# Kernel optimization log

Measured on AMD Instinct MI355X. Metric: run time of the kernel, lower is better.

## Reference

```python
import jax, jax.numpy as jnp
import numpy as np

NUM_LAYERS = 6
DIM = 512
VOCAB = 50257
HEADS = 8
EXPERTS = 8
TOPK = 2
LN_EPS = 1e-5


def setup_inputs() -> dict:
    key = jax.random.key(0)
    ks = jax.random.split(key, 9)
    d, L, E = DIM, NUM_LAYERS, EXPERTS
    return {
        'input_ids': jax.random.randint(ks[0], (2, 1024), 0, VOCAB),
        'embed': jax.random.normal(ks[1], (VOCAB, d), dtype=jnp.float32) * 0.02,
        'qkv_w': jax.random.normal(ks[2], (L, 3 * d, d), dtype=jnp.float32) * 0.02,
        'out_w': jax.random.normal(ks[3], (L, d, d), dtype=jnp.float32) * 0.02,
        'router_w': jax.random.normal(ks[4], (L, E, d), dtype=jnp.float32) * 0.02,
        'router_b': jnp.zeros((L, E), dtype=jnp.float32),
        'w1': jax.random.normal(ks[5], (L, E, 2 * d, d), dtype=jnp.float32) * 0.02,
        'b1': jnp.zeros((L, E, 2 * d), dtype=jnp.float32),
        'w2': jax.random.normal(ks[6], (L, E, d, 2 * d), dtype=jnp.float32) * 0.02,
        'b2': jnp.zeros((L, E, d), dtype=jnp.float32),
        'ln_g': jnp.ones((L, d), dtype=jnp.float32),
        'ln_b': jnp.zeros((L, d), dtype=jnp.float32),
        'head_w': jax.random.normal(ks[7], (VOCAB, d), dtype=jnp.float32) * 0.02,
    }


def _bit_weight(w):
    # BitNet 1.58b training-mode effective weight (STE forward value):
    # scale = mean|w| per output row; w_eff = round(w/scale).clip(-1,1) * scale
    scale = jnp.clip(jnp.mean(jnp.abs(w), axis=-1, keepdims=True), 1e-5, None)
    wq = jnp.clip(jnp.round(w / scale), -1.0, 1.0)
    w_ste = jax.lax.stop_gradient(wq - w) + w
    return w_ste * scale


def _layer_norm(x, g, b):
    mu = jnp.mean(x, axis=-1, keepdims=True)
    var = jnp.mean(jnp.square(x - mu), axis=-1, keepdims=True)
    return (x - mu) * jax.lax.rsqrt(var + LN_EPS) * g + b


def _attention(x, qkv_w, out_w):
    B, Lq, D = x.shape
    hd = D // HEADS
    qkv = (x @ qkv_w.T).reshape(B, Lq, 3, HEADS, hd).transpose(2, 0, 3, 1, 4)
    q, k, v = qkv[0], qkv[1], qkv[2]  # [B,H,L,hd]
    attn = jax.nn.softmax(jnp.einsum('bhqd,bhkd->bhqk', q, k) * hd ** -0.5, axis=-1)
    o = jnp.einsum('bhqk,bhkd->bhqd', attn, v).transpose(0, 2, 1, 3).reshape(B, Lq, D)
    return o @ out_w.T


def _moe(x, rw, rb, w1, b1, w2, b2, g, beta):
    B, Lq, D = x.shape
    N = B * Lq
    xf = x.reshape(N, D)
    probs = jax.nn.softmax(xf @ rw.T + rb, axis=-1)  # [N,E]
    vals, idx = jax.lax.top_k(probs, TOPK)
    vals = vals / (jnp.sum(vals, axis=-1, keepdims=True) + 1e-8)
    # combine weights: [N,E] (top-k indices are distinct, so sum == scatter)
    cw = jnp.sum(jax.nn.one_hot(idx, EXPERTS, dtype=xf.dtype) * vals[..., None], axis=1)
    we1 = _bit_weight(w1)  # [E,2D,D]
    we2 = _bit_weight(w2)  # [E,D,2D]
    h = jax.nn.gelu(jnp.einsum('nd,efd->enf', xf, we1) + b1[:, None, :], approximate=False)
    y = jnp.einsum('enf,edf->end', h, we2) + b2[:, None, :]  # [E,N,D]
    out = jnp.einsum('ne,end->nd', cw, y)
    return _layer_norm(out + xf, g, beta).reshape(B, Lq, D)


def reference(input_ids, embed, qkv_w, out_w, router_w, router_b, w1, b1, w2, b2, ln_g, ln_b, head_w):
    x = embed[input_ids]  # [B,L,D]
    for l in range(NUM_LAYERS):
        x = x + _attention(x, qkv_w[l], out_w[l])
        x = _moe(x, router_w[l], router_b[l], w1[l], b1[l], w2[l], b2[l], ln_g[l], ln_b[l])
    return x @ head_w.T  # logits [B,L,V]
```

## Files before the change

kernel.cpp:

```cpp
#include <hip/hip_runtime.h>
#include <math.h>
#include <stdint.h>

#define NLAYER 6
#define DIMD 512
#define HEADS 8
#define HD 64
#define EXPERTS 8
#define SEQ 1024
#define NTOK 2048
#define FF 1024
#define VOCABN 50257
#define HROWS 50304

typedef __bf16 bf16;
typedef __bf16 bf16x8 __attribute__((ext_vector_type(8)));
typedef __bf16 bf16x4 __attribute__((ext_vector_type(4)));
typedef float f32x4 __attribute__((ext_vector_type(4)));

__device__ __forceinline__ void gl_lds16(const void* g, void* l) {
  __builtin_amdgcn_global_load_lds(
      (const __attribute__((address_space(1))) void*)(uintptr_t)g,
      (__attribute__((address_space(3))) void*)(uintptr_t)l, 16, 0, 0);
}

#define LDSW(row, kg) (((row) * 32) + ((((kg) ^ (((row) >> 1) & 3))) << 3))

template <int BNT>
__global__ __launch_bounds__(256) void k_mfma_gemm(
    const bf16* __restrict__ A0, const bf16* __restrict__ A1,
    const bf16* __restrict__ B0, const bf16* __restrict__ B1,
    float* __restrict__ Cf, bf16* __restrict__ Cb0, bf16* __restrict__ Cb1,
    bf16* __restrict__ Cb2, bf16* __restrict__ E0, bf16* __restrict__ E1,
    bf16* __restrict__ E2, int M, int N, int K,
    long sA, long sB, long sCf, long sCb,
    const float* __restrict__ colScale, int csStride,
    const float* __restrict__ bias, int biasStride,
    const float* __restrict__ residual, int act, int mode,
    const int* __restrict__ mLimit, const int* __restrict__ aperm,
    int outmode) {
  constexpr int NI = BNT / 32;
  __shared__ __align__(16) bf16 As[128 * 32];
  __shared__ __align__(16) bf16 Bs[BNT * 32];
  int tid = threadIdx.x;
  int z = blockIdx.z;
  int nwg = gridDim.x * gridDim.y;
  int flat = blockIdx.y * gridDim.x + blockIdx.x;
  int qq = nwg >> 3, rr = nwg & 7;
  int xcd = flat & 7, ii = flat >> 3;
  int swz = (xcd < rr ? xcd * (qq + 1) : rr * (qq + 1) + (xcd - rr) * qq) + ii;
  int m0 = (swz % gridDim.x) * 128, n0 = (swz / gridDim.x) * BNT;
  if (mLimit && m0 >= mLimit[z]) return;
  int w = tid >> 6, lane = tid & 63;
  int wm = (w >> 1) * 64, wn = (w & 1) * (16 * NI);
  int r15 = lane & 15, kg = lane >> 4;

  int pa[3] = {0, 0, 0}, pb[3] = {0, 0, 0};
  int np = 1;
  if (mode == 3) {
    np = 2; pa[1] = 1;
  } else if (mode == 5) {
    np = 3;
    pa[1] = 0; pb[1] = 1; pa[2] = 1; pb[2] = 0;
  }

  f32x4 acc[4][NI] = {};
  int srow = tid >> 2;
  int scol = (((tid & 3) ^ ((tid >> 3) & 3))) << 3;
  long arow0, arow1;
  if (aperm) {
    arow0 = aperm[z * 2048 + m0 + srow];
    arow1 = aperm[z * 2048 + m0 + 64 + srow];
  } else {
    arow0 = m0 + srow;
    arow1 = m0 + 64 + srow;
  }
  const bf16* PA[2] = {A0, A1};
  const bf16* PB[2] = {B0, B1};
  bf16* la0 = &As[tid * 8];
  bf16* la1 = &As[64 * 32 + tid * 8];
  bf16* lb0 = &Bs[tid * 8];

  for (int p = 0; p < np; ++p) {
    const bf16* Az = PA[pa[p]] + (long)z * sA;
    const bf16* Bz = PB[pb[p]] + (long)z * sB;
    const bf16* ga0 = Az + arow0 * K + scol;
    const bf16* ga1 = Az + arow1 * K + scol;
    const bf16* gb0 = Bz + (long)(n0 + srow) * K + scol;
    const bf16* gb1 = (BNT == 128) ? Bz + (long)(n0 + 64 + srow) * K + scol
                                   : nullptr;
    for (int k0 = 0; k0 < K; k0 += 32) {
      gl_lds16(ga0, la0);
      gl_lds16(ga1, la1);
      gl_lds16(gb0, lb0);
      if constexpr (BNT == 128) gl_lds16(gb1, &Bs[64 * 32 + tid * 8]);
      ga0 += 32; ga1 += 32; gb0 += 32;
      if constexpr (BNT == 128) gb1 += 32;
      __syncthreads();
      bf16x8 af[4], bfr[NI];
#pragma unroll
      for (int mi = 0; mi < 4; ++mi) {
        int rowA = wm + mi * 16 + r15;
        af[mi] = *(const bf16x8*)&As[LDSW(rowA, kg)];
      }
#pragma unroll
      for (int ni = 0; ni < NI; ++ni) {
        int rowB = wn + ni * 16 + r15;
        bfr[ni] = *(const bf16x8*)&Bs[LDSW(rowB, kg)];
      }
#pragma unroll
      for (int mi = 0; mi < 4; ++mi)
#pragma unroll
        for (int ni = 0; ni < NI; ++ni)
          acc[mi][ni] = __builtin_amdgcn_mfma_f32_16x16x32_bf16(
              af[mi], bfr[ni], acc[mi][ni], 0, 0, 0);
      __syncthreads();
    }
  }

#pragma unroll
  for (int mi = 0; mi < 4; ++mi) {
    int rbase = m0 + wm + mi * 16 + kg * 4;
#pragma unroll
    for (int ni = 0; ni < NI; ++ni) {
      int col = n0 + wn + ni * 16 + r15;
      if (col >= N) continue;
      float scl = colScale ? colScale[z * csStride + col] : 1.f;
      float bv = bias ? bias[z * biasStride + col] : 0.f;
#pragma unroll
      for (int reg = 0; reg < 4; ++reg) {
        int row = rbase + reg;
        float v = acc[mi][ni][reg] * scl + bv;
        if (act) v = 0.5f * v * (1.f + erff(v * 0.70710678118654752f));
        if (residual) v += residual[(long)row * N + col];
        if (outmode == 2) {
          int b = row >> 10, qt = row & 1023;
          if (n0 < 512) {
            float qv = v * 0.125f;
            int h = col >> 6, d = col & 63;
            long dst = ((long)(b * 8 + h)) * ((long)SEQ * HD) +
                       (long)qt * HD + d;
            bf16 h0 = (bf16)qv;
            Cb0[dst] = h0;
            Cb1[dst] = (bf16)(qv - (float)h0);
          } else if (n0 < 1024) {
            int c2 = col - 512;
            int h = c2 >> 6, d = c2 & 63;
            long dst = ((long)(b * 8 + h)) * ((long)SEQ * HD) +
                       (long)qt * HD + d;
            bf16 h0 = (bf16)v;
            Cb2[dst] = h0;
            E0[dst] = (bf16)(v - (float)h0);
          } else {
            int c2 = col - 1024;
            int h = c2 >> 6, d = c2 & 63;
            long dst = ((long)(b * 8 + h)) * ((long)HD * SEQ) +
                       (long)d * SEQ + qt;
            bf16 h0 = (bf16)v;
            E1[dst] = h0;
            E2[dst] = (bf16)(v - (float)h0);
          }
          continue;
        }
        if (Cf) Cf[z * sCf + (long)row * N + col] = v;
        if (Cb0) {
          long cib = z * sCb + (long)row * N + col;
          bf16 h0 = (bf16)v;
          Cb0[cib] = h0;
          if (Cb1) {
            float r = v - (float)h0;
            Cb1[cib] = (bf16)r;
          }
        }
      }
    }
  }
}

__global__ __launch_bounds__(256) void k_fattn(
    const bf16* __restrict__ q0b, const bf16* __restrict__ q1b,
    const bf16* __restrict__ k0b, const bf16* __restrict__ k1b,
    const bf16* __restrict__ vt0, const bf16* __restrict__ vt1,
    bf16* __restrict__ at0, bf16* __restrict__ at1) {
  __shared__ __align__(16) bf16 Ks[2][128 * 64];
  __shared__ __align__(16) bf16 Vs[2][64 * 128];
  __shared__ __align__(16) bf16 Ps[2][64 * 128];
  int tid = threadIdx.x;
  int bh = blockIdx.y;
  int q0 = blockIdx.x * 64;
  int w = tid >> 6, lane = tid & 63;
  int r15 = lane & 15, kg = lane >> 4;
  const long bhQK = (long)bh * SEQ * HD;
  const long bhV = (long)bh * HD * SEQ;

  bf16x8 qa0[2], qa1[2];
  {
    long qoff = bhQK + (long)(q0 + w * 16 + r15) * HD;
#pragma unroll
    for (int ks = 0; ks < 2; ++ks) {
      qa0[ks] = *(const bf16x8*)&q0b[qoff + ks * 32 + kg * 8];
      qa1[ks] = *(const bf16x8*)&q1b[qoff + ks * 32 + kg * 8];
    }
  }

  auto stageK = [&](int kt) {
#pragma unroll
    for (int i = 0; i < 4; ++i) {
      int L = tid + i * 256;
      int row = L >> 3, pc = L & 7;
      int gc = pc ^ (row & 7);
      long gsrc = bhQK + (long)(kt * 128 + row) * HD + gc * 8;
      gl_lds16(k0b + gsrc, &Ks[0][L * 8]);
      gl_lds16(k1b + gsrc, &Ks[1][L * 8]);
    }
  };
  auto stageV = [&](int kt) {
#pragma unroll
    for (int i = 0; i < 4; ++i) {
      int L = tid + i * 256;
      int row = L >> 4, pc = L & 15;
      int gc = pc ^ (row & 15);
      long gsrc = bhV + (long)row * SEQ + kt * 128 + gc * 8;
      gl_lds16(vt0 + gsrc, &Vs[0][L * 8]);
      gl_lds16(vt1 + gsrc, &Vs[1][L * 8]);
    }
  };
  auto computeS = [&](f32x4* sf) {
#pragma unroll
    for (int kc = 0; kc < 8; ++kc) {
      f32x4 a = {};
      int rowB = kc * 16 + r15;
#pragma unroll
      for (int ks = 0; ks < 2; ++ks) {
        int pc = (ks * 4 + kg) ^ (rowB & 7);
        bf16x8 b0 = *(const bf16x8*)&Ks[0][rowB * 64 + pc * 8];
        bf16x8 b1 = *(const bf16x8*)&Ks[1][rowB * 64 + pc * 8];
        a = __builtin_amdgcn_mfma_f32_16x16x32_bf16(qa0[ks], b0, a, 0, 0, 0);
        a = __builtin_amdgcn_mfma_f32_16x16x32_bf16(qa0[ks], b1, a, 0, 0, 0);
        a = __builtin_amdgcn_mfma_f32_16x16x32_bf16(qa1[ks], b0, a, 0, 0, 0);
      }
      sf[kc] = a;
    }
  };

  float m[4], l[4];
#pragma unroll
  for (int r = 0; r < 4; ++r) { m[r] = -1e30f; l[r] = 0.f; }
  f32x4 oacc[4] = {};

  for (int kt = 0; kt < SEQ / 128; ++kt) {
    stageK(kt);
    stageV(kt);
    __syncthreads();
    f32x4 sf[8];
    computeS(sf);
#pragma unroll
    for (int r = 0; r < 4; ++r) {
      float tm = sf[0][r];
#pragma unroll
      for (int kc = 1; kc < 8; ++kc) tm = fmaxf(tm, sf[kc][r]);
      tm = fmaxf(tm, __shfl_xor(tm, 1));
      tm = fmaxf(tm, __shfl_xor(tm, 2));
      tm = fmaxf(tm, __shfl_xor(tm, 4));
      tm = fmaxf(tm, __shfl_xor(tm, 8));
      float mn = fmaxf(m[r], tm);
      float corr = __expf(m[r] - mn);
      float s = 0.f;
#pragma unroll
      for (int kc = 0; kc < 8; ++kc) {
        float p = __expf(sf[kc][r] - mn);
        sf[kc][r] = p;
        s += p;
      }
      s += __shfl_xor(s, 1);
      s += __shfl_xor(s, 2);
      s += __shfl_xor(s, 4);
      s += __shfl_xor(s, 8);
      l[r] = l[r] * corr + s;
      m[r] = mn;
#pragma unroll
      for (int dg = 0; dg < 4; ++dg) oacc[dg][r] *= corr;
    }
#pragma unroll
    for (int kc = 0; kc < 8; ++kc) {
#pragma unroll
      for (int r = 0; r < 4; ++r) {
        float p = sf[kc][r];
        bf16 h0 = (bf16)p;
        bf16 h1 = (bf16)(p - (float)h0);
        int qrow = w * 16 + kg * 4 + r;
        int kcol = kc * 16 + r15;
        int pc = (kcol >> 3) ^ (qrow & 15);
        int addr = qrow * 128 + pc * 8 + (kcol & 7);
        Ps[0][addr] = h0;
        Ps[1][addr] = h1;
      }
    }
    bf16x8 pa0[4], pa1[4];
    int rowP = w * 16 + r15;
#pragma unroll
    for (int ks = 0; ks < 4; ++ks) {
      int pc = (ks * 4 + kg) ^ (rowP & 15);
      pa0[ks] = *(const bf16x8*)&Ps[0][rowP * 128 + pc * 8];
      pa1[ks] = *(const bf16x8*)&Ps[1][rowP * 128 + pc * 8];
    }
#pragma unroll
    for (int dg = 0; dg < 4; ++dg) {
      int rowV = dg * 16 + r15;
#pragma unroll
      for (int ks = 0; ks < 4; ++ks) {
        int pc = (ks * 4 + kg) ^ (rowV & 15);
        bf16x8 v0 = *(const bf16x8*)&Vs[0][rowV * 128 + pc * 8];
        bf16x8 v1 = *(const bf16x8*)&Vs[1][rowV * 128 + pc * 8];
        oacc[dg] = __builtin_amdgcn_mfma_f32_16x16x32_bf16(pa0[ks], v0,
                                                           oacc[dg], 0, 0, 0);
        oacc[dg] = __builtin_amdgcn_mfma_f32_16x16x32_bf16(pa0[ks], v1,
                                                           oacc[dg], 0, 0, 0);
        oacc[dg] = __builtin_amdgcn_mfma_f32_16x16x32_bf16(pa1[ks], v0,
                                                           oacc[dg], 0, 0, 0);
      }
    }
    __syncthreads();
  }

  float invl[4];
#pragma unroll
  for (int r = 0; r < 4; ++r) invl[r] = 1.f / l[r];

  int b = bh >> 3, h = bh & 7;
#pragma unroll
  for (int dg = 0; dg < 4; ++dg) {
#pragma unroll
    for (int r = 0; r < 4; ++r) {
      int qrow = q0 + w * 16 + kg * 4 + r;
      int d = dg * 16 + r15;
      long dst = ((long)(b * SEQ + qrow)) * DIMD + h * HD + d;
      float v = oacc[dg][r] * invl[r];
      bf16 h0 = (bf16)v;
      at0[dst] = h0;
      at1[dst] = (bf16)(v - (float)h0);
    }
  }
}

__global__ __launch_bounds__(256) void k_hgemm(const bf16* __restrict__ A,
                                               const bf16* __restrict__ Bt,
                                               float* __restrict__ C,
                                               int M, int N, int K) {
  __shared__ __align__(16) bf16 As[128 * 64];
  __shared__ __align__(16) bf16 Bs[128 * 64];
  int tid = threadIdx.x;
  int nwg = gridDim.x * gridDim.y;
  int flat = blockIdx.y * gridDim.x + blockIdx.x;
  int qq = nwg >> 3, rr = nwg & 7;
  int xcd = flat & 7, ii = flat >> 3;
  int swz = (xcd < rr ? xcd * (qq + 1) : rr * (qq + 1) + (xcd - rr) * qq) + ii;
  int m0 = (swz % gridDim.x) * 128, n0 = (swz / gridDim.x) * 128;
  int w = tid >> 6, lane = tid & 63;
  int wm = (w >> 1) * 64, wn = (w & 1) * 64;
  int r15 = lane & 15, kg = lane >> 4;
  int srow = tid >> 3;
  int scol = (((tid & 7) ^ ((tid >> 3) & 7))) << 3;
  const bf16* ga = A + (long)(m0 + srow) * K + scol;
  const bf16* gb = Bt + (long)(n0 + srow) * K + scol;
  f32x4 acc[4][4] = {};
  for (int k0 = 0; k0 < K; k0 += 64) {
#pragma unroll
    for (int i = 0; i < 4; ++i) {
      gl_lds16(ga + (long)i * 32 * K + k0, &As[i * 2048 + tid * 8]);
      gl_lds16(gb + (long)i * 32 * K + k0, &Bs[i * 2048 + tid * 8]);
    }
    __syncthreads();
#pragma unroll
    for (int kk = 0; kk < 2; ++kk) {
      bf16x8 af[4], bf_[4];
#pragma unroll
      for (int mi = 0; mi < 4; ++mi) {
        int rowA = wm + mi * 16 + r15;
        af[mi] = *(const bf16x8*)
            &As[rowA * 64 + ((((kk * 4 + kg) ^ (rowA & 7))) << 3)];
      }
#pragma unroll
      for (int ni = 0; ni < 4; ++ni) {
        int rowB = wn + ni * 16 + r15;
        bf_[ni] = *(const bf16x8*)
            &Bs[rowB * 64 + ((((kk * 4 + kg) ^ (rowB & 7))) << 3)];
      }
#pragma unroll
      for (int mi = 0; mi < 4; ++mi)
#pragma unroll
        for (int ni = 0; ni < 4; ++ni)
          acc[mi][ni] = __builtin_amdgcn_mfma_f32_16x16x32_bf16(
              af[mi], bf_[ni], acc[mi][ni], 0, 0, 0);
    }
    __syncthreads();
  }
#pragma unroll
  for (int mi = 0; mi < 4; ++mi) {
    int rbase = m0 + wm + mi * 16 + kg * 4;
#pragma unroll
    for (int ni = 0; ni < 4; ++ni) {
      int col = n0 + wn + ni * 16 + r15;
      if (col >= N) continue;
#pragma unroll
      for (int reg = 0; reg < 4; ++reg)
        C[(long)(rbase + reg) * N + col] = acc[mi][ni][reg];
    }
  }
}

__global__ __launch_bounds__(256) void k_embed(const int* __restrict__ ids,
                                               const float* __restrict__ E,
                                               float* __restrict__ xf,
                                               bf16* __restrict__ x0,
                                               bf16* __restrict__ x1) {
  int i = blockIdx.x * 256 + threadIdx.x;
  if (i >= NTOK * DIMD) return;
  int n = i >> 9, d = i & 511;
  float v = E[(long)ids[n] * DIMD + d];
  xf[i] = v;
  bf16 b0 = (bf16)v;
  x0[i] = b0;
  x1[i] = (bf16)(v - (float)b0);
}

__global__ __launch_bounds__(256) void k_prepw(const float* __restrict__ qkv_w,
                                               const float* __restrict__ out_w,
                                               bf16* __restrict__ qw0a,
                                               bf16* __restrict__ qw1a,
                                               bf16* __restrict__ ow0a,
                                               bf16* __restrict__ ow1a) {
  int l = blockIdx.y;
  const long n8q = (long)3 * DIMD * DIMD / 8;
  long i = (long)blockIdx.x * 256 + threadIdx.x;
  const float* s;
  bf16 *d0, *d1;
  long j;
  if (i < n8q) {
    s = qkv_w + (long)l * 3 * DIMD * DIMD;
    d0 = qw0a + (long)l * 3 * DIMD * DIMD;
    d1 = qw1a + (long)l * 3 * DIMD * DIMD;
    j = i;
  } else {
    s = out_w + (long)l * DIMD * DIMD;
    d0 = ow0a + (long)l * DIMD * DIMD;
    d1 = ow1a + (long)l * DIMD * DIMD;
    j = i - n8q;
  }
  const float4* s4 = (const float4*)s;
  float4 a = s4[2 * j], b = s4[2 * j + 1];
  float vv[8] = {a.x, a.y, a.z, a.w, b.x, b.y, b.z, b.w};
  bf16x8 o0, o1;
#pragma unroll
  for (int k = 0; k < 8; ++k) {
    float v = vv[k];
    bf16 h0 = (bf16)v;
    o0[k] = h0;
    o1[k] = (bf16)(v - (float)h0);
  }
  ((bf16x8*)d0)[j] = o0;
  ((bf16x8*)d1)[j] = o1;
}

__global__ __launch_bounds__(256) void k_headconv(const float* __restrict__ s,
                                                  bf16* __restrict__ d) {
  long i = (long)blockIdx.x * 256 + threadIdx.x;
  long n8 = (long)HROWS * DIMD / 8;
  if (i >= n8) return;
  long row = i / (DIMD / 8);
  bf16x8 o;
  if (row < VOCABN) {
    const float4* s4 = (const float4*)s;
    float4 a = s4[2 * i], b = s4[2 * i + 1];
    o[0] = (bf16)a.x; o[1] = (bf16)a.y; o[2] = (bf16)a.z; o[3] = (bf16)a.w;
    o[4] = (bf16)b.x; o[5] = (bf16)b.y; o[6] = (bf16)b.z; o[7] = (bf16)b.w;
  } else {
    o = (bf16x8)(bf16)0.f;
  }
  ((bf16x8*)d)[i] = o;
}

__global__ __launch_bounds__(64) void k_router(const float* __restrict__ x,
                                               const float* __restrict__ rw,
                                               const float* __restrict__ rb,
                                               int* __restrict__ top2,
                                               float* __restrict__ v2) {
  int n = blockIdx.x;
  int t = threadIdx.x;
  int e = t >> 3, part = t & 7;
  __shared__ float red[64];
  const float* xr = x + (long)n * DIMD;
  const float* wr = rw + (long)e * DIMD;
  float d = 0.f;
  int c0 = part * 64;
#pragma unroll
  for (int c = 0; c < 64; c += 4) {
    float4 xv = *(const float4*)(xr + c0 + c);
    float4 wv = *(const float4*)(wr + c0 + c);
    d += xv.x * wv.x + xv.y * wv.y + xv.z * wv.z + xv.w * wv.w;
  }
  red[t] = d;
  __syncthreads();
  if (t < 8) {
    float logit = rb[t];
    for (int pp = 0; pp < 8; ++pp) logit += red[t * 8 + pp];
    red[t] = logit;
  }
  __syncthreads();
  if (t == 0) {
    float p2[8];
    float m = -1e30f;
    for (int i = 0; i < 8; ++i) m = fmaxf(m, red[i]);
    float s = 0.f;
    for (int i = 0; i < 8; ++i) { p2[i] = expf(red[i] - m); s += p2[i]; }
    for (int i = 0; i < 8; ++i) p2[i] /= s;
    int i1 = 0;
    for (int i = 1; i < 8; ++i) if (p2[i] > p2[i1]) i1 = i;
    int i2 = (i1 == 0) ? 1 : 0;
    for (int i = 0; i < 8; ++i) {
      if (i == i1 || i == i2) continue;
      if (p2[i] > p2[i2]) i2 = i;
    }
    float sum = p2[i1] + p2[i2] + 1e-8f;
    top2[2 * n] = i1;
    top2[2 * n + 1] = i2;
    v2[2 * n] = p2[i1] / sum;
    v2[2 * n + 1] = p2[i2] / sum;
  }
}

__global__ __launch_bounds__(256) void k_expcnt(const int* __restrict__ top2,
                                                int* __restrict__ perm,
                                                int* __restrict__ tokpos,
                                                int* __restrict__ cnt,
                                                bf16* __restrict__ zx0,
                                                bf16* __restrict__ zx1) {
  int e = blockIdx.x, t = threadIdx.x;
  if (e == 0) {
    for (int c = t; c < DIMD; c += 256) {
      zx0[c] = (bf16)0.f;
      zx1[c] = (bf16)0.f;
    }
  }
  __shared__ int sc[256];
  int fl[8];
  int f = 0;
#pragma unroll
  for (int j = 0; j < 8; ++j) {
    int n = t * 8 + j;
    int m = (top2[2 * n] == e || top2[2 * n + 1] == e) ? 1 : 0;
    fl[j] = m;
    f += m;
  }
  sc[t] = f;
  __syncthreads();
  for (int o = 1; o < 256; o <<= 1) {
    int v = (t >= o) ? sc[t - o] : 0;
    __syncthreads();
    sc[t] += v;
    __syncthreads();
  }
  int pos = sc[t] - f;
#pragma unroll
  for (int j = 0; j < 8; ++j) {
    if (fl[j]) {
      int n = t * 8 + j;
      perm[e * 2048 + pos] = n;
      int jj = (top2[2 * n] == e) ? 0 : 1;
      tokpos[2 * n + jj] = e * 2048 + pos;
      ++pos;
    }
  }
  int total = sc[255];
  int cpad = (total + 127) & ~127;
  for (int i = total + t; i < cpad; i += 256) perm[e * 2048 + i] = 2048;
  if (t == 0) cnt[e] = total;
}

__global__ __launch_bounds__(256) void k_bitw2(const float* __restrict__ w1,
                                               const float* __restrict__ w2,
                                               bf16* __restrict__ we1qa,
                                               float* __restrict__ s1a,
                                               bf16* __restrict__ we2qa,
                                               float* __restrict__ s2a) {
  int l = blockIdx.y;
  int blk = blockIdx.x;
  int t = threadIdx.x;
  const float* wr;
  bf16* outr;
  float* sOut;
  int cols;
  if (blk < EXPERTS * FF) {
    cols = DIMD;
    wr = w1 + (long)l * EXPERTS * FF * DIMD + (long)blk * cols;
    outr = we1qa + (long)l * EXPERTS * FF * DIMD + (long)blk * cols;
    sOut = s1a + (long)l * EXPERTS * FF + blk;
  } else {
    int row = blk - EXPERTS * FF;
    cols = FF;
    wr = w2 + (long)l * EXPERTS * DIMD * FF + (long)row * cols;
    outr = we2qa + (long)l * EXPERTS * DIMD * FF + (long)row * cols;
    sOut = s2a + (long)l * EXPERTS * DIMD + row;
  }
  float acc = 0.f;
  for (int c = t; c < cols; c += 256) acc += fabsf(wr[c]);
  __shared__ float red[256];
  red[t] = acc;
  __syncthreads();
  for (int off = 128; off; off >>= 1) {
    if (t < off) red[t] += red[t + off];
    __syncthreads();
  }
  float scale = fmaxf(red[0] / (float)cols, 1e-5f);
  if (t == 0) *sOut = scale;
  for (int c = t; c < cols; c += 256) {
    float qv = rintf(wr[c] / scale);
    qv = fmaxf(-1.f, fminf(1.f, qv));
    outr[c] = (bf16)qv;
  }
}

__global__ __launch_bounds__(128) void k_lncomb(
    const float* __restrict__ yg, const int* __restrict__ tokpos,
    const float* __restrict__ v2, const float* __restrict__ xBf,
    const float* __restrict__ g, const float* __restrict__ b,
    float* __restrict__ xof, bf16* __restrict__ x0, bf16* __restrict__ x1) {
  int n = blockIdx.x;
  int t = threadIdx.x;
  __shared__ float red[128];
  long tp0 = tokpos[2 * n], tp1 = tokpos[2 * n + 1];
  float w0 = v2[2 * n], w1 = v2[2 * n + 1];
  const float* y0 = yg + tp0 * DIMD;
  const float* y1 = yg + tp1 * DIMD;
  float u[4];
  float s = 0.f;
#pragma unroll
  for (int i = 0; i < 4; ++i) {
    int d = t + i * 128;
    float v = xBf[(long)n * DIMD + d] + w0 * y0[d] + w1 * y1[d];
    u[i] = v;
    s += v;
  }
  red[t] = s;
  __syncthreads();
  for (int off = 64; off; off >>= 1) {
    if (t < off) red[t] += red[t + off];
    __syncthreads();
  }
  float mu = red[0] / (float)DIMD;
  __syncthreads();
  float var = 0.f;
#pragma unroll
  for (int i = 0; i < 4; ++i) {
    float d = u[i] - mu;
    var += d * d;
  }
  red[t] = var;
  __syncthreads();
  for (int off = 64; off; off >>= 1) {
    if (t < off) red[t] += red[t + off];
    __syncthreads();
  }
  float inv = 1.f / sqrtf(red[0] / (float)DIMD + 1e-5f);
#pragma unroll
  for (int i = 0; i < 4; ++i) {
    int c = t + i * 128;
    float v = (u[i] - mu) * inv * g[c] + b[c];
    long oi = (long)n * DIMD + c;
    xof[oi] = v;
    bf16 b0 = (bf16)v;
    x0[oi] = b0;
    x1[oi] = (bf16)(v - (float)b0);
  }
}

extern "C" void kernel_launch(void* const* d_in, const int* in_sizes, int n_in,
                              void* d_out, int out_size, void* d_ws, size_t ws_size,
                              hipStream_t stream) {
  const int* ids = (const int*)d_in[0];
  const float* embed = (const float*)d_in[1];
  const float* qkv_w = (const float*)d_in[2];
  const float* out_w = (const float*)d_in[3];
  const float* router_w = (const float*)d_in[4];
  const float* router_b = (const float*)d_in[5];
  const float* w1 = (const float*)d_in[6];
  const float* b1 = (const float*)d_in[7];
  const float* w2 = (const float*)d_in[8];
  const float* b2 = (const float*)d_in[9];
  const float* ln_g = (const float*)d_in[10];
  const float* ln_b = (const float*)d_in[11];
  const float* head_w = (const float*)d_in[12];
  float* out = (float*)d_out;

  char* base = (char*)d_ws;
  size_t off = 0;
  auto alloc = [&](size_t bytes) -> void* {
    void* p = base + off;
    off += (bytes + 255) & ~(size_t)255;
    return p;
  };
  const size_t ND = (size_t)NTOK * DIMD;
  float* xAf = (float*)alloc(ND * 4);
  float* xBf = (float*)alloc(ND * 4);
  int* top2 = (int*)alloc((size_t)NTOK * 2 * 4);
  float* v2 = (float*)alloc((size_t)NTOK * 2 * 4);
  int* perm = (int*)alloc((size_t)EXPERTS * 2048 * 4);
  int* tokpos = (int*)alloc((size_t)NTOK * 2 * 4);
  int* cntb = (int*)alloc(64);
  bf16* xA0 = (bf16*)alloc(ND * 2);
  bf16* xA1 = (bf16*)alloc(ND * 2);
  bf16* xB0 = (bf16*)alloc((ND + DIMD) * 2);
  bf16* xB1 = (bf16*)alloc((ND + DIMD) * 2);
  bf16* at0 = (bf16*)alloc(ND * 2);
  bf16* at1 = (bf16*)alloc(ND * 2);
  bf16* q0b = (bf16*)alloc((size_t)16 * SEQ * HD * 2);
  bf16* q1b = (bf16*)alloc((size_t)16 * SEQ * HD * 2);
  bf16* k0b = (bf16*)alloc((size_t)16 * SEQ * HD * 2);
  bf16* k1b = (bf16*)alloc((size_t)16 * SEQ * HD * 2);
  bf16* vt0b = (bf16*)alloc((size_t)16 * HD * SEQ * 2);
  bf16* vt1b = (bf16*)alloc((size_t)16 * HD * SEQ * 2);
  bf16* qw0a = (bf16*)alloc((size_t)NLAYER * 3 * DIMD * DIMD * 2);
  bf16* qw1a = (bf16*)alloc((size_t)NLAYER * 3 * DIMD * DIMD * 2);
  bf16* ow0a = (bf16*)alloc((size_t)NLAYER * DIMD * DIMD * 2);
  bf16* ow1a = (bf16*)alloc((size_t)NLAYER * DIMD * DIMD * 2);
  bf16* we1qa = (bf16*)alloc((size_t)NLAYER * EXPERTS * FF * DIMD * 2);
  float* s1a = (float*)alloc((size_t)NLAYER * EXPERTS * FF * 4);
  bf16* we2qa = (bf16*)alloc((size_t)NLAYER * EXPERTS * DIMD * FF * 2);
  float* s2a = (float*)alloc((size_t)NLAYER * EXPERTS * DIMD * 4);

  size_t Ustart = off;
  bf16* h0g = (bf16*)alloc((size_t)EXPERTS * 2048 * FF * 2);
  bf16* h1g = (bf16*)alloc((size_t)EXPERTS * 2048 * FF * 2);
  float* yg = (float*)alloc((size_t)EXPERTS * 2048 * DIMD * 4);
  size_t endB = off;
  size_t endC = Ustart + (size_t)HROWS * DIMD * 2;
  bf16* hw0 = (bf16*)(base + Ustart);
  off = endB > endC ? endB : endC;
  if (ws_size < off) return;

  k_embed<<<(NTOK * DIMD + 255) / 256, 256, 0, stream>>>(ids, embed, xAf, xA0,
                                                         xA1);
  k_prepw<<<dim3(512, NLAYER), 256, 0, stream>>>(qkv_w, out_w, qw0a, qw1a,
                                                 ow0a, ow1a);
  k_bitw2<<<dim3(EXPERTS * FF + EXPERTS * DIMD, NLAYER), 256, 0, stream>>>(
      w1, w2, we1qa, s1a, we2qa, s2a);

  for (int l = 0; l < NLAYER; ++l) {
    bf16* qw0 = qw0a + (long)l * 3 * DIMD * DIMD;
    bf16* qw1 = qw1a + (long)l * 3 * DIMD * DIMD;
    bf16* ow0 = ow0a + (long)l * DIMD * DIMD;
    bf16* ow1 = ow1a + (long)l * DIMD * DIMD;
    bf16* we1q = we1qa + (long)l * EXPERTS * FF * DIMD;
    bf16* we2q = we2qa + (long)l * EXPERTS * DIMD * FF;
    float* s1 = s1a + (long)l * EXPERTS * FF;
    float* s2 = s2a + (long)l * EXPERTS * DIMD;
    k_mfma_gemm<128><<<dim3(NTOK / 128, (3 * DIMD) / 128, 1), 256, 0,
                       stream>>>(
        xA0, xA1, qw0, qw1, nullptr, q0b, q1b, k0b, k1b, vt0b, vt1b,
        NTOK, 3 * DIMD, DIMD, 0, 0, 0, 0,
        nullptr, 0, nullptr, 0, nullptr, 0, 5, nullptr, nullptr, 2);
    k_fattn<<<dim3(SEQ / 64, 16), 256, 0, stream>>>(q0b, q1b, k0b, k1b,
                                                    vt0b, vt1b, at0, at1);
    k_mfma_gemm<128><<<dim3(NTOK / 128, DIMD / 128, 1), 256, 0, stream>>>(
        at0, at1, ow0, ow1, xBf, xB0, xB1, nullptr, nullptr, nullptr,
        nullptr, NTOK, DIMD, DIMD, 0, 0, 0, 0,
        nullptr, 0, nullptr, 0, xAf, 0, 5, nullptr, nullptr, 0);
    k_router<<<NTOK, 64, 0, stream>>>(xBf, router_w + (long)l * EXPERTS * DIMD,
                                      router_b + l * EXPERTS, top2, v2);
    k_expcnt<<<EXPERTS, 256, 0, stream>>>(top2, perm, tokpos, cntb,
                                          xB0 + ND, xB1 + ND);
    k_mfma_gemm<128><<<dim3(NTOK / 128, FF / 128, EXPERTS), 256, 0, stream>>>(
        xB0, xB1, we1q, nullptr, nullptr, h0g, h1g, nullptr, nullptr, nullptr,
        nullptr, NTOK, FF, DIMD, 0, (long)FF * DIMD, 0, (long)2048 * FF,
        s1, FF, b1 + (long)l * EXPERTS * FF, FF, nullptr, 1, 3, cntb, perm, 0);
    k_mfma_gemm<128><<<dim3(NTOK / 128, DIMD / 128, EXPERTS), 256, 0,
                       stream>>>(
        h0g, h1g, we2q, nullptr, yg, nullptr, nullptr, nullptr, nullptr,
        nullptr, nullptr, NTOK, DIMD, FF, (long)2048 * FF, (long)DIMD * FF,
        (long)2048 * DIMD, 0, s2, DIMD, b2 + (long)l * EXPERTS * DIMD, DIMD,
        nullptr, 0, 3, cntb, nullptr, 0);
    k_lncomb<<<NTOK, 128, 0, stream>>>(yg, tokpos, v2, xBf, ln_g + l * DIMD,
                                       ln_b + l * DIMD, xAf, xA0, xA1);
  }
  long nh8 = (long)HROWS * DIMD / 8;
  k_headconv<<<(int)((nh8 + 255) / 256), 256, 0, stream>>>(head_w, hw0);
  k_hgemm<<<dim3(NTOK / 128, HROWS / 128, 1), 256, 0, stream>>>(
      xA0, hw0, out, NTOK, VOCABN, DIMD);
}
```

Before: 2.309 ms.

## Enlarge LM-head GEMM tiles to 256x256 with double-buffered LDS pipeline

Rewrites the vocabulary-projection GEMM to use 256x256 output tiles with 512 threads (8 waves, each computing 128x64), and double-buffers the LDS staging so the loads for tile k+2 overlap compute on tile k, with explicit vmcnt waits and barriers. Padding of the head weight rows is increased so the row count divides evenly by 256. The intent is more operand reuse per byte loaded and hidden global-load latency in the largest GEMM. In exchange it uses 128KB of LDS per block and more accumulator registers, and the fully unrolled K loop hardcodes K=512.

Result: faster. 2.257 ms (-2.3%).

```diff
diff --git a/kernel.cpp b/kernel.cpp
--- a/kernel.cpp
+++ b/kernel.cpp
@@ -11,7 +11,7 @@
 #define NTOK 2048
 #define FF 1024
 #define VOCABN 50257
-#define HROWS 50304
+#define HROWS 50432
 
 typedef __bf16 bf16;
 typedef __bf16 bf16x8 __attribute__((ext_vector_type(8)));
@@ -343,60 +343,82 @@
   }
 }
 
-__global__ __launch_bounds__(256) void k_hgemm(const bf16* __restrict__ A,
-                                               const bf16* __restrict__ Bt,
-                                               float* __restrict__ C,
-                                               int M, int N, int K) {
-  __shared__ __align__(16) bf16 As[128 * 64];
-  __shared__ __align__(16) bf16 Bs[128 * 64];
+__global__ __launch_bounds__(512, 2) void k_hgemm(const bf16* __restrict__ A,
+                                                  const bf16* __restrict__ Bt,
+                                                  float* __restrict__ C,
+                                                  int M, int N, int K) {
+  __shared__ __align__(16) bf16 As[2][256 * 64];
+  __shared__ __align__(16) bf16 Bs[2][256 * 64];
   int tid = threadIdx.x;
   int nwg = gridDim.x * gridDim.y;
   int flat = blockIdx.y * gridDim.x + blockIdx.x;
   int qq = nwg >> 3, rr = nwg & 7;
   int xcd = flat & 7, ii = flat >> 3;
   int swz = (xcd < rr ? xcd * (qq + 1) : rr * (qq + 1) + (xcd - rr) * qq) + ii;
-  int m0 = (swz % gridDim.x) * 128, n0 = (swz / gridDim.x) * 128;
+  int m0 = (swz % gridDim.x) * 256, n0 = (swz / gridDim.x) * 256;
   int w = tid >> 6, lane = tid & 63;
-  int wm = (w >> 1) * 64, wn = (w & 1) * 64;
+  int wm = (w >> 2) * 128, wn = (w & 3) * 64;
   int r15 = lane & 15, kg = lane >> 4;
-  int srow = tid >> 3;
-  int scol = (((tid & 7) ^ ((tid >> 3) & 7))) << 3;
-  const bf16* ga = A + (long)(m0 + srow) * K + scol;
-  const bf16* gb = Bt + (long)(n0 + srow) * K + scol;
-  f32x4 acc[4][4] = {};
-  for (int k0 = 0; k0 < K; k0 += 64) {
-#pragma unroll
-    for (int i = 0; i < 4; ++i) {
-      gl_lds16(ga + (long)i * 32 * K + k0, &As[i * 2048 + tid * 8]);
-      gl_lds16(gb + (long)i * 32 * K + k0, &Bs[i * 2048 + tid * 8]);
-    }
-    __syncthreads();
-#pragma unroll
-    for (int kk = 0; kk < 2; ++kk) {
-      bf16x8 af[4], bf_[4];
-#pragma unroll
-      for (int mi = 0; mi < 4; ++mi) {
-        int rowA = wm + mi * 16 + r15;
+
+  auto stage = [&](int buf, int kt) {
+#pragma unroll
+    for (int j = 0; j < 4; ++j) {
+      int L = tid + j * 512;
+      int row = L >> 3, pc = L & 7;
+      int gc = pc ^ (row & 7);
+      gl_lds16(A + (long)(m0 + row) * K + kt * 64 + gc * 8, &As[buf][L * 8]);
+      gl_lds16(Bt + (long)(n0 + row) * K + kt * 64 + gc * 8, &Bs[buf][L * 8]);
+    }
+  };
+
+  f32x4 acc[8][4] = {};
+  auto compute = [&](int buf) {
+#pragma unroll
+    for (int ks = 0; ks < 2; ++ks) {
+      bf16x8 af[8], bf_[4];
+#pragma unroll
+      for (int mi = 0; mi < 8; ++mi) {
+        int row = wm + mi * 16 + r15;
         af[mi] = *(const bf16x8*)
-            &As[rowA * 64 + ((((kk * 4 + kg) ^ (rowA & 7))) << 3)];
+            &As[buf][row * 64 + ((((ks * 4 + kg) ^ (row & 7))) << 3)];
       }
 #pragma unroll
       for (int ni = 0; ni < 4; ++ni) {
-        int rowB = wn + ni * 16 + r15;
+        int row = wn + ni * 16 + r15;
         bf_[ni] = *(const bf16x8*)
-            &Bs[rowB * 64 + ((((kk * 4 + kg) ^ (rowB & 7))) << 3)];
+            &Bs[buf][row * 64 + ((((ks * 4 + kg) ^ (row & 7))) << 3)];
       }
 #pragma unroll
-      for (int mi = 0; mi < 4; ++mi)
+      for (int mi = 0; mi < 8; ++mi)
 #pragma unroll
         for (int ni = 0; ni < 4; ++ni)
           acc[mi][ni] = __builtin_amdgcn_mfma_f32_16x16x32_bf16(
               af[mi], bf_[ni], acc[mi][ni], 0, 0, 0);
     }
-    __syncthreads();
-  }
-#pragma unroll
-  for (int mi = 0; mi < 4; ++mi) {
+  };
+
+  stage(0, 0);
+  stage(1, 1);
+#pragma unroll 1
+  for (int t = 0; t < 6; ++t) {
+    asm volatile("s_waitcnt vmcnt(8)" ::: "memory");
+    __builtin_amdgcn_s_barrier();
+    __builtin_amdgcn_sched_barrier(0);
+    compute(t & 1);
+    __builtin_amdgcn_s_barrier();
+    stage(t & 1, t + 2);
+  }
+  asm volatile("s_waitcnt vmcnt(8)" ::: "memory");
+  __builtin_amdgcn_s_barrier();
+  __builtin_amdgcn_sched_barrier(0);
+  compute(0);
+  asm volatile("s_waitcnt vmcnt(0)" ::: "memory");
+  __builtin_amdgcn_s_barrier();
+  __builtin_amdgcn_sched_barrier(0);
+  compute(1);
+
+#pragma unroll
+  for (int mi = 0; mi < 8; ++mi) {
     int rbase = m0 + wm + mi * 16 + kg * 4;
 #pragma unroll
     for (int ni = 0; ni < 4; ++ni) {
@@ -784,6 +806,6 @@
   }
   long nh8 = (long)HROWS * DIMD / 8;
   k_headconv<<<(int)((nh8 + 255) / 256), 256, 0, stream>>>(head_w, hw0);
-  k_hgemm<<<dim3(NTOK / 128, HROWS / 128, 1), 256, 0, stream>>>(
+  k_hgemm<<<dim3(NTOK / 256, HROWS / 256, 1), 512, 0, stream>>>(
       xA0, hw0, out, NTOK, VOCABN, DIMD);
 }
```
